# Performance work log

Hardware: AMD Instinct MI355X
Metric: run time of the kernel (lower is better)

Reference implementation:

```python
import jax, jax.numpy as jnp
import numpy as np

D_MODEL = 2048
D_INNER = 4096  # d_model * expand_factor
LN_EPS = 1e-5


def setup_inputs() -> dict:
    key = jax.random.key(0)
    k1, k2, k3, k4 = jax.random.split(key, 4)
    B, S = 2, 4096
    x = jax.random.normal(k1, (B, S, D_MODEL), dtype=jnp.float32)
    gamma = jnp.ones((D_MODEL,), dtype=jnp.float32)
    beta = jnp.zeros((D_MODEL,), dtype=jnp.float32)
    # nn.Linear-like small init to keep activations in-range
    W_in = jax.random.normal(k2, (2 * D_INNER, D_MODEL), dtype=jnp.float32) * 0.02
    W_out = jax.random.normal(k3, (D_MODEL, D_INNER), dtype=jnp.float32) * 0.02
    dt_min, dt_max = 0.001, 0.1
    dt = jax.random.uniform(k4, (D_INNER,), dtype=jnp.float32) * (dt_max - dt_min) + dt_min
    return {"x": x, "gamma": gamma, "beta": beta, "W_in": W_in, "W_out": W_out, "dt": dt}


def reference(x, gamma, beta, W_in, W_out, dt):
    # x: [B, S, D_MODEL]
    identity = x
    # LayerNorm over last dim
    mu = jnp.mean(x, axis=-1, keepdims=True)
    var = jnp.mean(jnp.square(x - mu), axis=-1, keepdims=True)
    xn = (x - mu) * jax.lax.rsqrt(var + LN_EPS) * gamma + beta
    # in_proj: [B, S, 2*D_INNER]
    projected = jnp.einsum("bsd,ed->bse", xn, W_in)
    z, gate = jnp.split(projected, 2, axis=-1)
    # z gated by sigmoid of clamped z (clamp only inside sigmoid)
    z_gated = z * jax.nn.sigmoid(jnp.clip(z, -15.0, 15.0))
    # temporal weighting by softmax(-dt) over d_inner
    dt_weights = jax.nn.softmax(-dt)  # [D_INNER]
    z_temporal = z_gated * dt_weights  # broadcast over [B, S, D_INNER]
    # gate path: silu on clamped gate
    output = z_temporal * jax.nn.silu(jnp.clip(gate, -15.0, 15.0))
    # out_proj back to d_model
    output = jnp.einsum("bse,de->bsd", output, W_out)
    return output + identity
```

## Files before the change

kernel.cpp:

```cpp
#include <hip/hip_runtime.h>
#include <cstdint>
#include <cstddef>

#define T_TOK 8192
#define DM    2048
#define DI    4096
#define TWO_DI 8192

typedef __attribute__((ext_vector_type(8))) short bf16x8;
typedef __attribute__((ext_vector_type(4))) float f32x4;

__device__ __forceinline__ unsigned short f2bf(float f) {
  union { float f; unsigned u; } c; c.f = f;
  unsigned u = c.u;
  unsigned r = (u + 0x7fffu + ((u >> 16) & 1u)) >> 16;
  return (unsigned short)r;
}
__device__ __forceinline__ float bf2f(unsigned short b) {
  union { unsigned u; float f; } c; c.u = ((unsigned)b) << 16;
  return c.f;
}

__global__ __launch_bounds__(256) void ln_kernel(
    const float* __restrict__ x, const float* __restrict__ gamma,
    const float* __restrict__ beta, unsigned short* __restrict__ xn) {
  const int t = blockIdx.x;
  const int tid = threadIdx.x;
  const float* row = x + (size_t)t * DM;
  float4 v0 = reinterpret_cast<const float4*>(row)[tid];
  float4 v1 = reinterpret_cast<const float4*>(row)[tid + 256];
  float s  = v0.x + v0.y + v0.z + v0.w + v1.x + v1.y + v1.z + v1.w;
  float ss = v0.x*v0.x + v0.y*v0.y + v0.z*v0.z + v0.w*v0.w
           + v1.x*v1.x + v1.y*v1.y + v1.z*v1.z + v1.w*v1.w;
  #pragma unroll
  for (int off = 32; off > 0; off >>= 1) {
    s  += __shfl_down(s, off);
    ss += __shfl_down(ss, off);
  }
  __shared__ float red[8];
  __shared__ float mu_s, inv_s;
  if ((tid & 63) == 0) { red[tid >> 6] = s; red[4 + (tid >> 6)] = ss; }
  __syncthreads();
  if (tid == 0) {
    float S  = red[0] + red[1] + red[2] + red[3];
    float SS = red[4] + red[5] + red[6] + red[7];
    float mu  = S * (1.0f / DM);
    float var = SS * (1.0f / DM) - mu * mu;
    mu_s = mu;
    inv_s = rsqrtf(var + 1e-5f);
  }
  __syncthreads();
  const float mu = mu_s, inv = inv_s;
  float4 g0 = reinterpret_cast<const float4*>(gamma)[tid];
  float4 b0 = reinterpret_cast<const float4*>(beta)[tid];
  float4 g1 = reinterpret_cast<const float4*>(gamma)[tid + 256];
  float4 b1 = reinterpret_cast<const float4*>(beta)[tid + 256];
  ushort4 o0, o1;
  o0.x = f2bf((v0.x - mu) * inv * g0.x + b0.x);
  o0.y = f2bf((v0.y - mu) * inv * g0.y + b0.y);
  o0.z = f2bf((v0.z - mu) * inv * g0.z + b0.z);
  o0.w = f2bf((v0.w - mu) * inv * g0.w + b0.w);
  o1.x = f2bf((v1.x - mu) * inv * g1.x + b1.x);
  o1.y = f2bf((v1.y - mu) * inv * g1.y + b1.y);
  o1.z = f2bf((v1.z - mu) * inv * g1.z + b1.z);
  o1.w = f2bf((v1.w - mu) * inv * g1.w + b1.w);
  reinterpret_cast<ushort4*>(xn + (size_t)t * DM)[tid]       = o0;
  reinterpret_cast<ushort4*>(xn + (size_t)t * DM)[tid + 256] = o1;
}

__global__ __launch_bounds__(256) void cvt_bf16(
    const float* __restrict__ in, unsigned short* __restrict__ out, int n4) {
  int i = blockIdx.x * 256 + threadIdx.x;
  if (i >= n4) return;
  float4 v = reinterpret_cast<const float4*>(in)[i];
  ushort4 o;
  o.x = f2bf(v.x); o.y = f2bf(v.y); o.z = f2bf(v.z); o.w = f2bf(v.w);
  reinterpret_cast<ushort4*>(out)[i] = o;
}

__global__ __launch_bounds__(256) void dt_softmax(
    const float* __restrict__ dt, float* __restrict__ w) {
  const int tid = threadIdx.x;
  float e[16];
  float local = 0.f;
  #pragma unroll
  for (int i = 0; i < 16; ++i) {
    float v = __expf(-dt[i * 256 + tid]);
    e[i] = v;
    local += v;
  }
  #pragma unroll
  for (int off = 32; off > 0; off >>= 1) local += __shfl_down(local, off);
  __shared__ float red[4];
  __shared__ float tot;
  if ((tid & 63) == 0) red[tid >> 6] = local;
  __syncthreads();
  if (tid == 0) tot = red[0] + red[1] + red[2] + red[3];
  __syncthreads();
  const float inv = 1.f / tot;
  #pragma unroll
  for (int i = 0; i < 16; ++i) w[i * 256 + tid] = e[i] * inv;
}

__device__ __forceinline__ float actf(float z, float g, float w) {
  float zc = fminf(fmaxf(z, -15.f), 15.f);
  float sz = 1.f / (1.f + __expf(-zc));
  float gc = fminf(fmaxf(g, -15.f), 15.f);
  float sg = 1.f / (1.f + __expf(-gc));
  return z * sz * w * gc * sg;
}

#define BM 128
#define BN 128
#define BK 64

__global__ __launch_bounds__(512, 2) void gemm1_fused(
    const unsigned short* __restrict__ A, const unsigned short* __restrict__ W,
    const float* __restrict__ dtw, unsigned short* __restrict__ act) {
  __shared__ unsigned short lds[3 * BM * BK];
  unsigned short* lA  = lds;
  unsigned short* lB1 = lds + BM * BK;
  unsigned short* lB2 = lds + 2 * BM * BK;
  float* Xbuf = reinterpret_cast<float*>(lds);

  const int tid  = threadIdx.x;
  const int lane = tid & 63;
  const int wave = tid >> 6;
  const int wq   = wave & 3;
  const int wm   = (wq >> 1) << 6;
  const int wn   = (wq & 1) << 6;
  const bool isZ = wave < 4;
  const int tM = blockIdx.y * BM;
  const int tN = blockIdx.x * BN;

  f32x4 acc[4][4];
  #pragma unroll
  for (int i = 0; i < 4; ++i)
    #pragma unroll
    for (int j = 0; j < 4; ++j) acc[i][j] = f32x4{0.f, 0.f, 0.f, 0.f};

  const unsigned short* Ab = A + (size_t)tM * DM;
  const unsigned short* B1 = W + (size_t)tN * DM;
  const unsigned short* B2 = W + (size_t)(tN + DI) * DM;
  const unsigned short* lB = isZ ? lB1 : lB2;

  for (int k0 = 0; k0 < DM; k0 += BK) {
    #pragma unroll
    for (int i = 0; i < 2; ++i) {
      const int t8  = i * 512 + tid;
      const int row = t8 >> 3;
      const int s8  = t8 & 7;
      const int col = ((s8 ^ (row & 7)) << 3);
      __builtin_amdgcn_global_load_lds(
          (const __attribute__((address_space(1))) void*)(Ab + (size_t)row * DM + k0 + col),
          (__attribute__((address_space(3))) void*)(&lA[t8 << 3]), 16, 0, 0);
      __builtin_amdgcn_global_load_lds(
          (const __attribute__((address_space(1))) void*)(B1 + (size_t)row * DM + k0 + col),
          (__attribute__((address_space(3))) void*)(&lB1[t8 << 3]), 16, 0, 0);
      __builtin_amdgcn_global_load_lds(
          (const __attribute__((address_space(1))) void*)(B2 + (size_t)row * DM + k0 + col),
          (__attribute__((address_space(3))) void*)(&lB2[t8 << 3]), 16, 0, 0);
    }
    __syncthreads();

    #pragma unroll
    for (int kk = 0; kk < BK; kk += 32) {
      const int r0 = lane & 15;
      const int s8 = (((kk >> 3) + (lane >> 4)) ^ (r0 & 7)) << 3;
      bf16x8 af[4], bfr[4];
      #pragma unroll
      for (int i = 0; i < 4; ++i)
        af[i] = *reinterpret_cast<const bf16x8*>(&lA[(wm + i * 16 + r0) * BK + s8]);
      #pragma unroll
      for (int j = 0; j < 4; ++j)
        bfr[j] = *reinterpret_cast<const bf16x8*>(&lB[(wn + j * 16 + r0) * BK + s8]);
      #pragma unroll
      for (int i = 0; i < 4; ++i)
        #pragma unroll
        for (int j = 0; j < 4; ++j)
          acc[i][j] = __builtin_amdgcn_mfma_f32_16x16x32_bf16(af[i], bfr[j], acc[i][j], 0, 0, 0);
    }
    __syncthreads();
  }

  const int c15 = lane & 15;
  const int qr  = (lane >> 4) << 2;

  if (wave == 4 || wave == 5) {
    #pragma unroll
    for (int i = 0; i < 4; ++i)
      #pragma unroll
      for (int r = 0; r < 4; ++r) {
        const int lr = i * 16 + qr + r;
        #pragma unroll
        for (int j = 0; j < 4; ++j)
          Xbuf[lr * 132 + wn + j * 16 + c15] = acc[i][j][r];
      }
  }
  __syncthreads();
  if (wave == 0 || wave == 1) {
    float w4[4];
    #pragma unroll
    for (int j = 0; j < 4; ++j) w4[j] = dtw[tN + wn + j * 16 + c15];
    #pragma unroll
    for (int i = 0; i < 4; ++i)
      #pragma unroll
      for (int r = 0; r < 4; ++r) {
        const int lr = i * 16 + qr + r;
        const size_t rowoff = (size_t)(tM + lr) * DI + tN + wn + c15;
        #pragma unroll
        for (int j = 0; j < 4; ++j) {
          const float g = Xbuf[lr * 132 + wn + j * 16 + c15];
          act[rowoff + j * 16] = f2bf(actf(acc[i][j][r], g, w4[j]));
        }
      }
  }
  __syncthreads();
  if (wave == 6 || wave == 7) {
    #pragma unroll
    for (int i = 0; i < 4; ++i)
      #pragma unroll
      for (int r = 0; r < 4; ++r) {
        const int lr = i * 16 + qr + r;
        #pragma unroll
        for (int j = 0; j < 4; ++j)
          Xbuf[lr * 132 + wn + j * 16 + c15] = acc[i][j][r];
      }
  }
  __syncthreads();
  if (wave == 2 || wave == 3) {
    float w4[4];
    #pragma unroll
    for (int j = 0; j < 4; ++j) w4[j] = dtw[tN + wn + j * 16 + c15];
    #pragma unroll
    for (int i = 0; i < 4; ++i)
      #pragma unroll
      for (int r = 0; r < 4; ++r) {
        const int lr = i * 16 + qr + r;
        const size_t rowoff = (size_t)(tM + 64 + lr) * DI + tN + wn + c15;
        #pragma unroll
        for (int j = 0; j < 4; ++j) {
          const float g = Xbuf[lr * 132 + wn + j * 16 + c15];
          act[rowoff + j * 16] = f2bf(actf(acc[i][j][r], g, w4[j]));
        }
      }
  }
}

__global__ __launch_bounds__(256, 2) void gemm_nt_res(
    const unsigned short* __restrict__ A, const unsigned short* __restrict__ Bm,
    float* __restrict__ Cf, const float* __restrict__ ident, int M, int N, int K) {
  __shared__ unsigned short lA[BM * BK];
  __shared__ unsigned short lB[BN * BK];
  const int tid  = threadIdx.x;
  const int lane = tid & 63;
  const int wave = tid >> 6;
  const int wm = (wave >> 1) << 6;
  const int wn = (wave & 1) << 6;
  const int tM = blockIdx.y * BM;
  const int tN = blockIdx.x * BN;

  f32x4 acc[4][4];
  #pragma unroll
  for (int i = 0; i < 4; ++i)
    #pragma unroll
    for (int j = 0; j < 4; ++j) acc[i][j] = f32x4{0.f, 0.f, 0.f, 0.f};

  const unsigned short* Ab = A + (size_t)tM * K;
  const unsigned short* Bb = Bm + (size_t)tN * K;

  for (int k0 = 0; k0 < K; k0 += BK) {
    #pragma unroll
    for (int i = 0; i < 4; ++i) {
      const int t8  = i * 256 + tid;
      const int row = t8 >> 3;
      const int s8  = t8 & 7;
      const int col = ((s8 ^ (row & 7)) << 3);
      __builtin_amdgcn_global_load_lds(
          (const __attribute__((address_space(1))) void*)(Ab + (size_t)row * K + k0 + col),
          (__attribute__((address_space(3))) void*)(&lA[t8 << 3]), 16, 0, 0);
      __builtin_amdgcn_global_load_lds(
          (const __attribute__((address_space(1))) void*)(Bb + (size_t)row * K + k0 + col),
          (__attribute__((address_space(3))) void*)(&lB[t8 << 3]), 16, 0, 0);
    }
    __syncthreads();

    #pragma unroll
    for (int kk = 0; kk < BK; kk += 32) {
      const int r0 = lane & 15;
      const int s8 = (((kk >> 3) + (lane >> 4)) ^ (r0 & 7)) << 3;
      bf16x8 af[4], bfr[4];
      #pragma unroll
      for (int i = 0; i < 4; ++i)
        af[i] = *reinterpret_cast<const bf16x8*>(&lA[(wm + i * 16 + r0) * BK + s8]);
      #pragma unroll
      for (int j = 0; j < 4; ++j)
        bfr[j] = *reinterpret_cast<const bf16x8*>(&lB[(wn + j * 16 + r0) * BK + s8]);
      #pragma unroll
      for (int i = 0; i < 4; ++i)
        #pragma unroll
        for (int j = 0; j < 4; ++j)
          acc[i][j] = __builtin_amdgcn_mfma_f32_16x16x32_bf16(af[i], bfr[j], acc[i][j], 0, 0, 0);
    }
    __syncthreads();
  }

  const int cn = tN + wn + (lane & 15);
  const int rm = tM + wm + ((lane >> 4) << 2);
  #pragma unroll
  for (int i = 0; i < 4; ++i) {
    #pragma unroll
    for (int r = 0; r < 4; ++r) {
      const size_t rowoff = (size_t)(rm + i * 16 + r) * N;
      #pragma unroll
      for (int j = 0; j < 4; ++j) {
        const size_t idx = rowoff + cn + j * 16;
        Cf[idx] = acc[i][j][r] + ident[idx];
      }
    }
  }
}

extern "C" void kernel_launch(void* const* d_in, const int* in_sizes, int n_in,
                              void* d_out, int out_size, void* d_ws, size_t ws_size,
                              hipStream_t stream) {
  const float* x     = (const float*)d_in[0];
  const float* gamma = (const float*)d_in[1];
  const float* beta  = (const float*)d_in[2];
  const float* W_in  = (const float*)d_in[3];
  const float* W_out = (const float*)d_in[4];
  const float* dt    = (const float*)d_in[5];
  float* out = (float*)d_out;

  char* ws = (char*)d_ws;
  unsigned short* xn     = (unsigned short*)(ws);
  unsigned short* win_b  = (unsigned short*)(ws + ((size_t)32 << 20));
  unsigned short* wout_b = (unsigned short*)(ws + ((size_t)64 << 20));
  float*          dtw    = (float*)(ws + ((size_t)80 << 20));
  unsigned short* act    = (unsigned short*)(ws + ((size_t)96 << 20));

  ln_kernel<<<T_TOK, 256, 0, stream>>>(x, gamma, beta, xn);
  cvt_bf16<<<(TWO_DI * DM / 4 + 255) / 256, 256, 0, stream>>>(W_in, win_b, TWO_DI * DM / 4);
  cvt_bf16<<<(DM * DI / 4 + 255) / 256, 256, 0, stream>>>(W_out, wout_b, DM * DI / 4);
  dt_softmax<<<1, 256, 0, stream>>>(dt, dtw);

  gemm1_fused<<<dim3(DI / BN, T_TOK / BM), 512, 0, stream>>>(xn, win_b, dtw, act);

  gemm_nt_res<<<dim3(DM / BN, T_TOK / BM), 256, 0, stream>>>(
      act, wout_b, out, x, T_TOK, DM, DI);
}
```

Baseline: 602.6 us.

## Compute z and gate tiles in same waves, drop LDS epilogue exchange; merge weight conversions

The fused in-projection GEMM moves from 8 waves (4 for z, 4 for gate) to 4 waves that each hold both z and gate accumulators. This lets the SiLU/sigmoid epilogue run straight from registers, with no LDS staging and no serialized sync phases. The cost is doubled accumulator registers per thread (128 floats for accumulators), which may cut occupancy or cause spills, and half as many threads issue the loads. The two weight-conversion launches are also merged into one kernel.

```diff
diff --git a/kernel.cpp b/kernel.cpp
--- a/kernel.cpp
+++ b/kernel.cpp
@@ -68,14 +68,19 @@
   reinterpret_cast<ushort4*>(xn + (size_t)t * DM)[tid + 256] = o1;
 }
 
-__global__ __launch_bounds__(256) void cvt_bf16(
-    const float* __restrict__ in, unsigned short* __restrict__ out, int n4) {
+__global__ __launch_bounds__(256) void cvt_both(
+    const float* __restrict__ a, unsigned short* __restrict__ oa, int n4a,
+    const float* __restrict__ b, unsigned short* __restrict__ ob, int n4b) {
   int i = blockIdx.x * 256 + threadIdx.x;
-  if (i >= n4) return;
-  float4 v = reinterpret_cast<const float4*>(in)[i];
+  const float* src;
+  unsigned short* dst;
+  int idx;
+  if (i < n4a) { src = a; dst = oa; idx = i; }
+  else { idx = i - n4a; if (idx >= n4b) return; src = b; dst = ob; }
+  float4 v = reinterpret_cast<const float4*>(src)[idx];
   ushort4 o;
   o.x = f2bf(v.x); o.y = f2bf(v.y); o.z = f2bf(v.z); o.w = f2bf(v.w);
-  reinterpret_cast<ushort4*>(out)[i] = o;
+  reinterpret_cast<ushort4*>(dst)[idx] = o;
 }
 
 __global__ __launch_bounds__(256) void dt_softmax(
@@ -114,51 +119,50 @@
 #define BN 128
 #define BK 64
 
-__global__ __launch_bounds__(512, 2) void gemm1_fused(
+__global__ __launch_bounds__(256, 2) void gemm1_fused(
     const unsigned short* __restrict__ A, const unsigned short* __restrict__ W,
     const float* __restrict__ dtw, unsigned short* __restrict__ act) {
-  __shared__ unsigned short lds[3 * BM * BK];
-  unsigned short* lA  = lds;
-  unsigned short* lB1 = lds + BM * BK;
-  unsigned short* lB2 = lds + 2 * BM * BK;
-  float* Xbuf = reinterpret_cast<float*>(lds);
+  __shared__ unsigned short lA[BM * BK];
+  __shared__ unsigned short lB1[BN * BK];
+  __shared__ unsigned short lB2[BN * BK];
 
   const int tid  = threadIdx.x;
   const int lane = tid & 63;
   const int wave = tid >> 6;
-  const int wq   = wave & 3;
-  const int wm   = (wq >> 1) << 6;
-  const int wn   = (wq & 1) << 6;
-  const bool isZ = wave < 4;
+  const int wm   = (wave >> 1) << 6;
+  const int wn   = (wave & 1) << 6;
   const int tM = blockIdx.y * BM;
   const int tN = blockIdx.x * BN;
 
-  f32x4 acc[4][4];
+  f32x4 accZ[4][4], accG[4][4];
   #pragma unroll
   for (int i = 0; i < 4; ++i)
     #pragma unroll
-    for (int j = 0; j < 4; ++j) acc[i][j] = f32x4{0.f, 0.f, 0.f, 0.f};
+    for (int j = 0; j < 4; ++j) {
+      accZ[i][j] = f32x4{0.f, 0.f, 0.f, 0.f};
+      accG[i][j] = f32x4{0.f, 0.f, 0.f, 0.f};
+    }
 
   const unsigned short* Ab = A + (size_t)tM * DM;
   const unsigned short* B1 = W + (size_t)tN * DM;
   const unsigned short* B2 = W + (size_t)(tN + DI) * DM;
-  const unsigned short* lB = isZ ? lB1 : lB2;
 
   for (int k0 = 0; k0 < DM; k0 += BK) {
     #pragma unroll
-    for (int i = 0; i < 2; ++i) {
-      const int t8  = i * 512 + tid;
+    for (int i = 0; i < 4; ++i) {
+      const int t8  = i * 256 + tid;
       const int row = t8 >> 3;
       const int s8  = t8 & 7;
       const int col = ((s8 ^ (row & 7)) << 3);
-      __builtin_amdgcn_global_load_lds(
-          (const __attribute__((address_space(1))) void*)(Ab + (size_t)row * DM + k0 + col),
+      const size_t goff = (size_t)row * DM + k0 + col;
+      __builtin_amdgcn_global_load_lds(
+          (const __attribute__((address_space(1))) void*)(Ab + goff),
           (__attribute__((address_space(3))) void*)(&lA[t8 << 3]), 16, 0, 0);
       __builtin_amdgcn_global_load_lds(
-          (const __attribute__((address_space(1))) void*)(B1 + (size_t)row * DM + k0 + col),
+          (const __attribute__((address_space(1))) void*)(B1 + goff),
           (__attribute__((address_space(3))) void*)(&lB1[t8 << 3]), 16, 0, 0);
       __builtin_amdgcn_global_load_lds(
-          (const __attribute__((address_space(1))) void*)(B2 + (size_t)row * DM + k0 + col),
+          (const __attribute__((address_space(1))) void*)(B2 + goff),
           (__attribute__((address_space(3))) void*)(&lB2[t8 << 3]), 16, 0, 0);
     }
     __syncthreads();
@@ -167,83 +171,40 @@
     for (int kk = 0; kk < BK; kk += 32) {
       const int r0 = lane & 15;
       const int s8 = (((kk >> 3) + (lane >> 4)) ^ (r0 & 7)) << 3;
-      bf16x8 af[4], bfr[4];
+      bf16x8 af[4], b1f[4], b2f[4];
       #pragma unroll
       for (int i = 0; i < 4; ++i)
         af[i] = *reinterpret_cast<const bf16x8*>(&lA[(wm + i * 16 + r0) * BK + s8]);
       #pragma unroll
-      for (int j = 0; j < 4; ++j)
-        bfr[j] = *reinterpret_cast<const bf16x8*>(&lB[(wn + j * 16 + r0) * BK + s8]);
+      for (int j = 0; j < 4; ++j) {
+        b1f[j] = *reinterpret_cast<const bf16x8*>(&lB1[(wn + j * 16 + r0) * BK + s8]);
+        b2f[j] = *reinterpret_cast<const bf16x8*>(&lB2[(wn + j * 16 + r0) * BK + s8]);
+      }
       #pragma unroll
       for (int i = 0; i < 4; ++i)
         #pragma unroll
-        for (int j = 0; j < 4; ++j)
-          acc[i][j] = __builtin_amdgcn_mfma_f32_16x16x32_bf16(af[i], bfr[j], acc[i][j], 0, 0, 0);
+        for (int j = 0; j < 4; ++j) {
+          accZ[i][j] = __builtin_amdgcn_mfma_f32_16x16x32_bf16(af[i], b1f[j], accZ[i][j], 0, 0, 0);
+          accG[i][j] = __builtin_amdgcn_mfma_f32_16x16x32_bf16(af[i], b2f[j], accG[i][j], 0, 0, 0);
+        }
     }
     __syncthreads();
   }
 
   const int c15 = lane & 15;
   const int qr  = (lane >> 4) << 2;
-
-  if (wave == 4 || wave == 5) {
-    #pragma unroll
-    for (int i = 0; i < 4; ++i)
-      #pragma unroll
-      for (int r = 0; r < 4; ++r) {
-        const int lr = i * 16 + qr + r;
-        #pragma unroll
-        for (int j = 0; j < 4; ++j)
-          Xbuf[lr * 132 + wn + j * 16 + c15] = acc[i][j][r];
-      }
-  }
-  __syncthreads();
-  if (wave == 0 || wave == 1) {
-    float w4[4];
-    #pragma unroll
-    for (int j = 0; j < 4; ++j) w4[j] = dtw[tN + wn + j * 16 + c15];
-    #pragma unroll
-    for (int i = 0; i < 4; ++i)
-      #pragma unroll
-      for (int r = 0; r < 4; ++r) {
-        const int lr = i * 16 + qr + r;
-        const size_t rowoff = (size_t)(tM + lr) * DI + tN + wn + c15;
-        #pragma unroll
-        for (int j = 0; j < 4; ++j) {
-          const float g = Xbuf[lr * 132 + wn + j * 16 + c15];
-          act[rowoff + j * 16] = f2bf(actf(acc[i][j][r], g, w4[j]));
-        }
-      }
-  }
-  __syncthreads();
-  if (wave == 6 || wave == 7) {
-    #pragma unroll
-    for (int i = 0; i < 4; ++i)
-      #pragma unroll
-      for (int r = 0; r < 4; ++r) {
-        const int lr = i * 16 + qr + r;
-        #pragma unroll
-        for (int j = 0; j < 4; ++j)
-          Xbuf[lr * 132 + wn + j * 16 + c15] = acc[i][j][r];
-      }
-  }
-  __syncthreads();
-  if (wave == 2 || wave == 3) {
-    float w4[4];
-    #pragma unroll
-    for (int j = 0; j < 4; ++j) w4[j] = dtw[tN + wn + j * 16 + c15];
-    #pragma unroll
-    for (int i = 0; i < 4; ++i)
-      #pragma unroll
-      for (int r = 0; r < 4; ++r) {
-        const int lr = i * 16 + qr + r;
-        const size_t rowoff = (size_t)(tM + 64 + lr) * DI + tN + wn + c15;
-        #pragma unroll
-        for (int j = 0; j < 4; ++j) {
-          const float g = Xbuf[lr * 132 + wn + j * 16 + c15];
-          act[rowoff + j * 16] = f2bf(actf(acc[i][j][r], g, w4[j]));
-        }
-      }
+  float w4[4];
+  #pragma unroll
+  for (int j = 0; j < 4; ++j) w4[j] = dtw[tN + wn + j * 16 + c15];
+  #pragma unroll
+  for (int i = 0; i < 4; ++i) {
+    #pragma unroll
+    for (int r = 0; r < 4; ++r) {
+      const size_t rowoff = (size_t)(tM + wm + i * 16 + qr + r) * DI + tN + wn + c15;
+      #pragma unroll
+      for (int j = 0; j < 4; ++j)
+        act[rowoff + j * 16] = f2bf(actf(accZ[i][j][r], accG[i][j][r], w4[j]));
+    }
   }
 }
 
@@ -339,12 +300,15 @@
   float*          dtw    = (float*)(ws + ((size_t)80 << 20));
   unsigned short* act    = (unsigned short*)(ws + ((size_t)96 << 20));
 
+  const int n4_in  = TWO_DI * DM / 4;
+  const int n4_out = DM * DI / 4;
+
   ln_kernel<<<T_TOK, 256, 0, stream>>>(x, gamma, beta, xn);
-  cvt_bf16<<<(TWO_DI * DM / 4 + 255) / 256, 256, 0, stream>>>(W_in, win_b, TWO_DI * DM / 4);
-  cvt_bf16<<<(DM * DI / 4 + 255) / 256, 256, 0, stream>>>(W_out, wout_b, DM * DI / 4);
+  cvt_both<<<(n4_in + n4_out + 255) / 256, 256, 0, stream>>>(
+      W_in, win_b, n4_in, W_out, wout_b, n4_out);
   dt_softmax<<<1, 256, 0, stream>>>(dt, dtw);
 
-  gemm1_fused<<<dim3(DI / BN, T_TOK / BM), 512, 0, stream>>>(xn, win_b, dtw, act);
+  gemm1_fused<<<dim3(DI / BN, T_TOK / BM), 256, 0, stream>>>(xn, win_b, dtw, act);
 
   gemm_nt_res<<<dim3(DM / BN, T_TOK / BM), 256, 0, stream>>>(
       act, wout_b, out, x, T_TOK, DM, DI);
```

After: 564.4 us. 1.07x faster.
